# Optimization experiments

Measured on AMD Instinct MI355X. Metric: run time of the kernel, lower is better.

## Reference

```python
import jax, jax.numpy as jnp
import numpy as np

V = 5023   # FLAME vertex count
NJ = 5     # joints: global, neck, jaw, left eye, right eye
PARENTS = [-1, 0, 1, 1, 1]
N_SHAPE, N_EXPR = 100, 50
N_LMK = 68
B = 1024


def batch_rodrigues(rot_vecs):
    # rot_vecs: [N,3] axis-angle -> [N,3,3] rotation matrices
    angle = jnp.linalg.norm(rot_vecs + 1e-8, axis=1, keepdims=True)  # [N,1]
    rot_dir = rot_vecs / angle
    cos = jnp.cos(angle)[:, :, None]  # [N,1,1]
    sin = jnp.sin(angle)[:, :, None]
    rx, ry, rz = rot_dir[:, 0], rot_dir[:, 1], rot_dir[:, 2]
    zeros = jnp.zeros_like(rx)
    K = jnp.stack([zeros, -rz, ry,
                   rz, zeros, -rx,
                   -ry, rx, zeros], axis=1).reshape(-1, 3, 3)
    ident = jnp.eye(3, dtype=rot_vecs.dtype)
    return ident[None] + sin * K + (1.0 - cos) * jnp.matmul(K, K)


def setup_inputs() -> dict:
    key = jax.random.key(0)
    ks = jax.random.split(key, 12)
    shape_params = jax.random.normal(ks[0], (B, N_SHAPE), jnp.float32)
    expression_params = jax.random.normal(ks[1], (B, N_EXPR), jnp.float32)
    pose_params = 0.2 * jax.random.normal(ks[2], (B, 6), jnp.float32)
    land_index = jax.random.randint(ks[3], (N_LMK,), 0, V)
    # buffers / params (stand-ins for the pickled FLAME model)
    v_template = jax.random.normal(ks[4], (V, 3), jnp.float32) * 100.0
    v_template = v_template - jnp.mean(v_template, axis=0, keepdims=True)  # init centering
    shapedirs = jax.random.normal(ks[5], (V, 3, N_SHAPE + N_EXPR), jnp.float32) * 0.1
    posedirs = jax.random.normal(ks[6], ((NJ - 1) * 9, V * 3), jnp.float32) * 0.01
    J_regressor = jax.nn.softmax(jax.random.normal(ks[7], (NJ, V), jnp.float32), axis=1)
    lbs_weights = jax.nn.softmax(jax.random.normal(ks[8], (V, NJ), jnp.float32), axis=1)
    eye_pose = jnp.zeros((1, 6), jnp.float32)
    neck_pose = jnp.zeros((1, 3), jnp.float32)
    return dict(shape_params=shape_params, expression_params=expression_params,
                pose_params=pose_params, land_index=land_index,
                v_template=v_template, shapedirs=shapedirs, posedirs=posedirs,
                J_regressor=J_regressor, lbs_weights=lbs_weights,
                eye_pose=eye_pose, neck_pose=neck_pose)


def lbs(betas, full_pose, v_template, shapedirs, posedirs, J_regressor, lbs_weights):
    b = betas.shape[0]
    # shape/expression blendshapes
    v_shaped = v_template[None] + jnp.einsum('bl,vcl->bvc', betas, shapedirs)  # [B,V,3]
    J = jnp.einsum('jv,bvc->bjc', J_regressor, v_shaped)                       # [B,5,3]
    rot_mats = batch_rodrigues(full_pose.reshape(-1, 3)).reshape(b, NJ, 3, 3)
    ident = jnp.eye(3, dtype=betas.dtype)
    pose_feature = (rot_mats[:, 1:] - ident).reshape(b, -1)                    # [B,36]
    v_posed = v_shaped + jnp.matmul(pose_feature, posedirs).reshape(b, V, 3)
    # rigid transform along kinematic chain
    rel_joints = J.at[:, 1:].add(-J[:, jnp.array(PARENTS[1:])])
    top = jnp.concatenate([rot_mats, rel_joints[..., None]], axis=-1)          # [B,5,3,4]
    bottom = jnp.broadcast_to(jnp.array([0., 0., 0., 1.], betas.dtype), (b, NJ, 1, 4))
    transforms_mat = jnp.concatenate([top, bottom], axis=2)                    # [B,5,4,4]
    chain = [transforms_mat[:, 0]]
    for i in range(1, NJ):
        chain.append(jnp.matmul(chain[PARENTS[i]], transforms_mat[:, i]))
    transforms = jnp.stack(chain, axis=1)                                      # [B,5,4,4]
    posed_joints = transforms[:, :, :3, 3]
    t = jnp.einsum('bnij,bnj->bni', transforms[:, :, :3, :3], J)
    rel_transforms = transforms.at[:, :, :3, 3].add(-t)
    # skinning
    T = jnp.einsum('vj,bjxy->bvxy', lbs_weights, rel_transforms)               # [B,V,4,4]
    verts = jnp.einsum('bvxy,bvy->bvx', T[:, :, :3, :3], v_posed) + T[:, :, :3, 3]
    return verts, posed_joints


def reference(shape_params, expression_params, pose_params, land_index,
              v_template, shapedirs, posedirs, J_regressor, lbs_weights,
              eye_pose, neck_pose):
    b = shape_params.shape[0]
    betas = jnp.concatenate([shape_params, expression_params], axis=1)
    full_pose = jnp.concatenate([pose_params[:, :3],
                                 jnp.broadcast_to(neck_pose, (b, 3)),
                                 pose_params[:, 3:],
                                 jnp.broadcast_to(eye_pose, (b, 6))], axis=1)  # [B,15]
    vertices, _ = lbs(betas, full_pose, v_template, shapedirs, posedirs,
                      J_regressor, lbs_weights)
    landmarks3d = jnp.take(vertices, land_index, axis=1)
    return vertices, landmarks3d
```

## Files before the change

### kernel.cpp

```cpp
#include <hip/hip_runtime.h>

#define V_N 5023
#define NC_REAL 15069
#define NC_PAD 15168
#define KTOT 192
#define B_N 1024

__device__ __forceinline__ float bf2f(unsigned short u) {
  union { unsigned int i; float f; } x; x.i = ((unsigned int)u) << 16; return x.f;
}
__device__ __forceinline__ unsigned short f2bf(float f) {
  union { float f; unsigned int i; } x; x.f = f;
  unsigned int u = x.i;
  u = (u + 0x7FFFu + ((u >> 16) & 1u)) >> 16;
  return (unsigned short)u;
}

__global__ void k_sd_transpose(const float* __restrict__ sd,
                               unsigned short* __restrict__ sdT) {
  __shared__ unsigned short tile[64][153];
  int vc0 = blockIdx.x * 64;
  int t = threadIdx.x;
  int col = t >> 2, q = t & 3;
  int vc = vc0 + col;
  #pragma unroll
  for (int i = 0; i < 38; ++i) {
    int k = q * 38 + i;
    unsigned short val = 0;
    if (k < 150 && vc < NC_REAL) val = f2bf(sd[vc * 150 + k]);
    tile[col][k] = val;
  }
  __syncthreads();
  for (int u = t; u < 152 * 32; u += 256) {
    int row = u >> 5, cp = u & 31;
    unsigned int lo = tile[2 * cp][row], hi = tile[2 * cp + 1][row];
    ((unsigned int*)sdT)[row * (NC_PAD / 2) + (vc0 >> 1) + cp] = lo | (hi << 16);
  }
}

__global__ void k_pd_copy(const float* __restrict__ pd,
                          unsigned short* __restrict__ sdT) {
  int g = blockIdx.x * 256 + threadIdx.x;
  int rr = g / NC_PAD, vc = g - rr * NC_PAD;
  unsigned short val = 0;
  if (rr < 36 && vc < NC_REAL) val = f2bf(pd[rr * NC_REAL + vc]);
  sdT[(152 + rr) * NC_PAD + vc] = val;
}

__global__ void k_js(const float* __restrict__ jreg,
                     const float* __restrict__ sd,
                     const float* __restrict__ vt,
                     float* __restrict__ JS, float* __restrict__ Jt) {
  int blk = blockIdx.x;
  int t = threadIdx.x;
  float acc[5] = {0.f, 0.f, 0.f, 0.f, 0.f};
  if (blk < 450) {
    int c = blk / 150, l = blk - (blk / 150) * 150;
    for (int v = t; v < V_N; v += 256) {
      float s = sd[(v * 3 + c) * 150 + l];
      #pragma unroll
      for (int j = 0; j < 5; j++) acc[j] += jreg[j * V_N + v] * s;
    }
  } else {
    int c = blk - 450;
    for (int v = t; v < V_N; v += 256) {
      float s = vt[v * 3 + c];
      #pragma unroll
      for (int j = 0; j < 5; j++) acc[j] += jreg[j * V_N + v] * s;
    }
  }
  __shared__ float red[5][4];
  #pragma unroll
  for (int j = 0; j < 5; j++) {
    float x = acc[j];
    for (int off = 32; off > 0; off >>= 1) x += __shfl_down(x, off);
    if ((t & 63) == 0) red[j][t >> 6] = x;
  }
  __syncthreads();
  if (t < 5) {
    float s = red[t][0] + red[t][1] + red[t][2] + red[t][3];
    if (blk < 450) {
      int c = blk / 150, l = blk - (blk / 150) * 150;
      JS[(t * 3 + c) * 150 + l] = s;
    } else {
      Jt[t * 3 + (blk - 450)] = s;
    }
  }
}

__global__ void k_betasT(const float* __restrict__ shp,
                         const float* __restrict__ expr,
                         float* __restrict__ betasT) {
  int g = blockIdx.x * 256 + threadIdx.x;
  int k = g >> 10, b = g & 1023;
  float v = 0.f;
  if (k < 100) v = shp[b * 100 + k];
  else if (k < 150) v = expr[b * 50 + (k - 100)];
  betasT[g] = v;
}

__device__ __forceinline__ void rodrigues(const float* p, float* R) {
  float x = p[0], y = p[1], z = p[2];
  float xa = x + 1e-8f, ya = y + 1e-8f, za = z + 1e-8f;
  float angle = sqrtf(xa * xa + ya * ya + za * za);
  float inv = 1.0f / angle;
  float rx = x * inv, ry = y * inv, rz = z * inv;
  float c = cosf(angle), s = sinf(angle), t1 = 1.0f - c;
  float K[9] = {0.f, -rz, ry, rz, 0.f, -rx, -ry, rx, 0.f};
  float KK[9];
  #pragma unroll
  for (int i = 0; i < 3; i++)
    #pragma unroll
    for (int j = 0; j < 3; j++) {
      float a = 0.f;
      #pragma unroll
      for (int k = 0; k < 3; k++) a += K[i * 3 + k] * K[k * 3 + j];
      KK[i * 3 + j] = a;
    }
  #pragma unroll
  for (int i = 0; i < 9; i++) R[i] = s * K[i] + t1 * KK[i];
  R[0] += 1.f; R[4] += 1.f; R[8] += 1.f;
}

__global__ void k_pose(const float* __restrict__ pose,
                       const float* __restrict__ neck,
                       const float* __restrict__ eye,
                       const float* __restrict__ JS,
                       const float* __restrict__ Jt,
                       float* __restrict__ betasT,
                       float* __restrict__ relT) {
  int b = blockIdx.x * 256 + threadIdx.x;
  if (b >= B_N) return;
  float fp[15];
  fp[0] = pose[b * 6 + 0]; fp[1] = pose[b * 6 + 1]; fp[2] = pose[b * 6 + 2];
  fp[3] = neck[0]; fp[4] = neck[1]; fp[5] = neck[2];
  fp[6] = pose[b * 6 + 3]; fp[7] = pose[b * 6 + 4]; fp[8] = pose[b * 6 + 5];
  #pragma unroll
  for (int i = 0; i < 6; i++) fp[9 + i] = eye[i];
  float R[5][9];
  #pragma unroll
  for (int j = 0; j < 5; j++) rodrigues(&fp[j * 3], R[j]);
  float J[5][3];
  #pragma unroll
  for (int j = 0; j < 5; j++)
    #pragma unroll
    for (int c = 0; c < 3; c++) J[j][c] = Jt[j * 3 + c];
  for (int k = 0; k < 150; k++) {
    float be = betasT[k * B_N + b];
    #pragma unroll
    for (int j = 0; j < 5; j++)
      #pragma unroll
      for (int c = 0; c < 3; c++) J[j][c] += be * JS[(j * 3 + c) * 150 + k];
  }
  float rel[5][3];
  #pragma unroll
  for (int c = 0; c < 3; c++) {
    rel[0][c] = J[0][c];
    rel[1][c] = J[1][c] - J[0][c];
    rel[2][c] = J[2][c] - J[1][c];
    rel[3][c] = J[3][c] - J[1][c];
    rel[4][c] = J[4][c] - J[1][c];
  }
  float GR[5][9], Gt[5][3];
  #pragma unroll
  for (int i = 0; i < 9; i++) GR[0][i] = R[0][i];
  #pragma unroll
  for (int c = 0; c < 3; c++) Gt[0][c] = rel[0][c];
  const int parent[5] = {0, 0, 1, 1, 1};
  #pragma unroll
  for (int j = 1; j < 5; j++) {
    int p = parent[j];
    #pragma unroll
    for (int r = 0; r < 3; r++)
      #pragma unroll
      for (int c = 0; c < 3; c++) {
        float a = 0.f;
        #pragma unroll
        for (int k = 0; k < 3; k++) a += GR[p][r * 3 + k] * R[j][k * 3 + c];
        GR[j][r * 3 + c] = a;
      }
    #pragma unroll
    for (int r = 0; r < 3; r++) {
      float a = Gt[p][r];
      #pragma unroll
      for (int k = 0; k < 3; k++) a += GR[p][r * 3 + k] * rel[j][k];
      Gt[j][r] = a;
    }
  }
  #pragma unroll
  for (int j = 0; j < 5; j++) {
    #pragma unroll
    for (int r = 0; r < 3; r++) {
      float a = 0.f;
      #pragma unroll
      for (int k = 0; k < 3; k++) a += GR[j][r * 3 + k] * J[j][k];
      float tr = Gt[j][r] - a;
      #pragma unroll
      for (int c = 0; c < 3; c++) relT[b * 60 + j * 12 + r * 4 + c] = GR[j][r * 3 + c];
      relT[b * 60 + j * 12 + r * 4 + 3] = tr;
    }
  }
  #pragma unroll
  for (int j = 1; j < 5; j++)
    #pragma unroll
    for (int r = 0; r < 3; r++)
      #pragma unroll
      for (int c = 0; c < 3; c++) {
        int kk = (j - 1) * 9 + r * 3 + c;
        betasT[(152 + kk) * B_N + b] = R[j][r * 3 + c] - ((r == c) ? 1.f : 0.f);
      }
  #pragma unroll
  for (int kk = 36; kk < 40; kk++) betasT[(152 + kk) * B_N + b] = 0.f;
}

__global__ __launch_bounds__(256) void k_main(
    const unsigned short* __restrict__ sdT,
    const float* __restrict__ betasT,
    const float* __restrict__ relT,
    const float* __restrict__ vt,
    const float* __restrict__ lbsw,
    float* __restrict__ out) {
  __shared__ float sBet[8][64];
  __shared__ float sSd[8][3][64];
  int t = threadIdx.x;
  int bg = t >> 5;
  int tv = t & 31;
  int v0 = blockIdx.x * 64;
  int b0 = blockIdx.y * 64;
  float acc[8][2][3];
  #pragma unroll
  for (int a = 0; a < 8; a++)
    #pragma unroll
    for (int b2 = 0; b2 < 2; b2++)
      #pragma unroll
      for (int c = 0; c < 3; c++) acc[a][b2][c] = 0.f;
  const unsigned int* sdT32 = (const unsigned int*)sdT;
  for (int kc = 0; kc < 24; kc++) {
    int k0 = kc * 8;
    {
      int f = t;
      #pragma unroll
      for (int i = 0; i < 2; i++, f += 256) {
        int r = f >> 6, c = f & 63;
        sBet[r][c] = betasT[(k0 + r) * B_N + b0 + c];
      }
      int u = t;
      #pragma unroll
      for (int i = 0; i < 3; i++, u += 256) {
        int r = u / 96, c2 = u - (u / 96) * 96;
        unsigned int w = sdT32[(k0 + r) * (NC_PAD / 2) + blockIdx.x * 96 + c2];
        int vcA = 2 * c2, vcB = vcA + 1;
        sSd[r][vcA % 3][vcA / 3] = bf2f((unsigned short)(w & 0xFFFFu));
        sSd[r][vcB % 3][vcB / 3] = bf2f((unsigned short)(w >> 16));
      }
    }
    __syncthreads();
    #pragma unroll
    for (int r = 0; r < 8; r++) {
      float4 be0 = *(const float4*)&sBet[r][bg * 8];
      float4 be1 = *(const float4*)&sBet[r][bg * 8 + 4];
      float2 sx = *(const float2*)&sSd[r][0][2 * tv];
      float2 sy = *(const float2*)&sSd[r][1][2 * tv];
      float2 sz = *(const float2*)&sSd[r][2][2 * tv];
      float be[8] = {be0.x, be0.y, be0.z, be0.w, be1.x, be1.y, be1.z, be1.w};
      #pragma unroll
      for (int bi = 0; bi < 8; bi++) {
        acc[bi][0][0] += be[bi] * sx.x;
        acc[bi][1][0] += be[bi] * sx.y;
        acc[bi][0][1] += be[bi] * sy.x;
        acc[bi][1][1] += be[bi] * sy.y;
        acc[bi][0][2] += be[bi] * sz.x;
        acc[bi][1][2] += be[bi] * sz.y;
      }
    }
    __syncthreads();
  }
  int vA = v0 + 2 * tv, vB = vA + 1;
  bool okA = vA < V_N, okB = vB < V_N;
  float vtA[3] = {0.f, 0.f, 0.f}, vtB[3] = {0.f, 0.f, 0.f};
  float wA[5] = {0.f, 0.f, 0.f, 0.f, 0.f}, wB[5] = {0.f, 0.f, 0.f, 0.f, 0.f};
  if (okA) {
    #pragma unroll
    for (int c = 0; c < 3; c++) vtA[c] = vt[vA * 3 + c];
    #pragma unroll
    for (int j = 0; j < 5; j++) wA[j] = lbsw[vA * 5 + j];
  }
  if (okB) {
    #pragma unroll
    for (int c = 0; c < 3; c++) vtB[c] = vt[vB * 3 + c];
    #pragma unroll
    for (int j = 0; j < 5; j++) wB[j] = lbsw[vB * 5 + j];
  }
  #pragma unroll
  for (int bi = 0; bi < 8; bi++) {
    int b = b0 + bg * 8 + bi;
    const float4* rT = (const float4*)(relT + b * 60);
    float pA0 = acc[bi][0][0] + vtA[0], pA1 = acc[bi][0][1] + vtA[1], pA2 = acc[bi][0][2] + vtA[2];
    float pB0 = acc[bi][1][0] + vtB[0], pB1 = acc[bi][1][1] + vtB[1], pB2 = acc[bi][1][2] + vtB[2];
    float oA0 = 0.f, oA1 = 0.f, oA2 = 0.f, oB0 = 0.f, oB1 = 0.f, oB2 = 0.f;
    #pragma unroll
    for (int j = 0; j < 5; j++) {
      float4 m0 = rT[j * 3 + 0], m1 = rT[j * 3 + 1], m2 = rT[j * 3 + 2];
      oA0 += wA[j] * (m0.x * pA0 + m0.y * pA1 + m0.z * pA2 + m0.w);
      oA1 += wA[j] * (m1.x * pA0 + m1.y * pA1 + m1.z * pA2 + m1.w);
      oA2 += wA[j] * (m2.x * pA0 + m2.y * pA1 + m2.z * pA2 + m2.w);
      oB0 += wB[j] * (m0.x * pB0 + m0.y * pB1 + m0.z * pB2 + m0.w);
      oB1 += wB[j] * (m1.x * pB0 + m1.y * pB1 + m1.z * pB2 + m1.w);
      oB2 += wB[j] * (m2.x * pB0 + m2.y * pB1 + m2.z * pB2 + m2.w);
    }
    if (okA) {
      size_t off = (size_t)b * NC_REAL + (size_t)vA * 3;
      out[off] = oA0; out[off + 1] = oA1; out[off + 2] = oA2;
    }
    if (okB) {
      size_t off = (size_t)b * NC_REAL + (size_t)vB * 3;
      out[off] = oB0; out[off + 1] = oB1; out[off + 2] = oB2;
    }
  }
}

__global__ void k_lmk(const float* __restrict__ verts,
                      const int* __restrict__ land,
                      float* __restrict__ lm) {
  int g = blockIdx.x * 256 + threadIdx.x;
  int b = g / 204;
  int r = g - b * 204;
  int i = r / 3, c = r - i * 3;
  lm[g] = verts[(size_t)b * NC_REAL + (size_t)land[i] * 3 + c];
}

extern "C" void kernel_launch(void* const* d_in, const int* in_sizes, int n_in,
                              void* d_out, int out_size, void* d_ws, size_t ws_size,
                              hipStream_t stream) {
  const float* shp  = (const float*)d_in[0];
  const float* expr = (const float*)d_in[1];
  const float* pose = (const float*)d_in[2];
  const int*   land = (const int*)d_in[3];
  const float* vt   = (const float*)d_in[4];
  const float* sd   = (const float*)d_in[5];
  const float* pd   = (const float*)d_in[6];
  const float* jreg = (const float*)d_in[7];
  const float* lbsw = (const float*)d_in[8];
  const float* eye  = (const float*)d_in[9];
  const float* neck = (const float*)d_in[10];
  char* ws = (char*)d_ws;
  unsigned short* sdT = (unsigned short*)(ws + 0);
  float* betasT = (float*)(ws + 5824512);
  float* JS     = (float*)(ws + 6610944);
  float* Jt     = (float*)(ws + 6620160);
  float* relT   = (float*)(ws + 6620224);
  float* outv = (float*)d_out;
  float* outl = outv + (size_t)B_N * NC_REAL;

  hipLaunchKernelGGL(k_sd_transpose, dim3(237), dim3(256), 0, stream, sd, sdT);
  hipLaunchKernelGGL(k_pd_copy, dim3(2370), dim3(256), 0, stream, pd, sdT);
  hipLaunchKernelGGL(k_js, dim3(453), dim3(256), 0, stream, jreg, sd, vt, JS, Jt);
  hipLaunchKernelGGL(k_betasT, dim3(608), dim3(256), 0, stream, shp, expr, betasT);
  hipLaunchKernelGGL(k_pose, dim3(4), dim3(256), 0, stream, pose, neck, eye, JS, Jt, betasT, relT);
  hipLaunchKernelGGL(k_main, dim3(79, 16), dim3(256), 0, stream, sdT, betasT, relT, vt, lbsw, outv);
  hipLaunchKernelGGL(k_lmk, dim3(816), dim3(256), 0, stream, outv, land, outl);
}
```

Baseline: 274.9 us.

## Move blendshape GEMM to bf16 MFMA and restructure preprocessing kernels

```diff
diff --git a/kernel.cpp b/kernel.cpp
--- a/kernel.cpp
+++ b/kernel.cpp
@@ -1,14 +1,22 @@
 #include <hip/hip_runtime.h>
 
 #define V_N 5023
-#define NC_REAL 15069
-#define NC_PAD 15168
+#define V_PAD 5120
 #define KTOT 192
 #define B_N 1024
-
-__device__ __forceinline__ float bf2f(unsigned short u) {
-  union { unsigned int i; float f; } x; x.i = ((unsigned int)u) << 16; return x.f;
-}
+#define NC_REAL 15069
+
+#define WS_W     0
+#define WS_A2    5898240
+#define WS_PART1 6291456
+#define WS_PARTJ 6561456
+#define WS_JS    6563264
+#define WS_JT    6572272
+#define WS_RELT  6572336
+
+typedef __attribute__((ext_vector_type(8))) short bf16x8;
+typedef __attribute__((ext_vector_type(4))) float f32x4;
+
 __device__ __forceinline__ unsigned short f2bf(float f) {
   union { float f; unsigned int i; } x; x.f = f;
   unsigned int u = x.i;
@@ -16,87 +24,82 @@
   return (unsigned short)u;
 }
 
-__global__ void k_sd_transpose(const float* __restrict__ sd,
-                               unsigned short* __restrict__ sdT) {
-  __shared__ unsigned short tile[64][153];
-  int vc0 = blockIdx.x * 64;
-  int t = threadIdx.x;
-  int col = t >> 2, q = t & 3;
-  int vc = vc0 + col;
-  #pragma unroll
-  for (int i = 0; i < 38; ++i) {
-    int k = q * 38 + i;
-    unsigned short val = 0;
-    if (k < 150 && vc < NC_REAL) val = f2bf(sd[vc * 150 + k]);
-    tile[col][k] = val;
-  }
-  __syncthreads();
-  for (int u = t; u < 152 * 32; u += 256) {
-    int row = u >> 5, cp = u & 31;
-    unsigned int lo = tile[2 * cp][row], hi = tile[2 * cp + 1][row];
-    ((unsigned int*)sdT)[row * (NC_PAD / 2) + (vc0 >> 1) + cp] = lo | (hi << 16);
-  }
-}
-
-__global__ void k_pd_copy(const float* __restrict__ pd,
-                          unsigned short* __restrict__ sdT) {
+__global__ void k_w2(const float* __restrict__ sd, const float* __restrict__ pd,
+                     unsigned short* __restrict__ W) {
+  int vc = blockIdx.x * 256 + threadIdx.x;
+  int v = vc / 3, c = vc - 3 * v;
+  unsigned short* dst = W + ((size_t)c * V_PAD + v) * KTOT;
+  if (vc < NC_REAL) {
+    for (int k = 0; k < 150; k++) dst[k] = f2bf(sd[(size_t)vc * 150 + k]);
+    dst[150] = 0; dst[151] = 0;
+    for (int kk = 0; kk < 36; kk++) dst[152 + kk] = f2bf(pd[(size_t)kk * NC_REAL + vc]);
+    for (int k = 188; k < 192; k++) dst[k] = 0;
+  } else {
+    for (int k = 0; k < 192; k++) dst[k] = 0;
+  }
+}
+
+__global__ void k_a2(const float* __restrict__ shp, const float* __restrict__ expr,
+                     unsigned short* __restrict__ A2) {
   int g = blockIdx.x * 256 + threadIdx.x;
-  int rr = g / NC_PAD, vc = g - rr * NC_PAD;
-  unsigned short val = 0;
-  if (rr < 36 && vc < NC_REAL) val = f2bf(pd[rr * NC_REAL + vc]);
-  sdT[(152 + rr) * NC_PAD + vc] = val;
-}
-
-__global__ void k_js(const float* __restrict__ jreg,
-                     const float* __restrict__ sd,
-                     const float* __restrict__ vt,
-                     float* __restrict__ JS, float* __restrict__ Jt) {
+  int b = g / 76, u = g - b * 76;
+  int k0 = 2 * u, k1 = 2 * u + 1;
+  float f0 = 0.f, f1 = 0.f;
+  if (k0 < 100) f0 = shp[b * 100 + k0]; else if (k0 < 150) f0 = expr[b * 50 + k0 - 100];
+  if (k1 < 100) f1 = shp[b * 100 + k1]; else if (k1 < 150) f1 = expr[b * 50 + k1 - 100];
+  unsigned int w = (unsigned int)f2bf(f0) | ((unsigned int)f2bf(f1) << 16);
+  ((unsigned int*)A2)[b * 96 + u] = w;
+}
+
+__global__ void k_js1(const float* __restrict__ jreg, const float* __restrict__ sd,
+                      const float* __restrict__ vt,
+                      float* __restrict__ part1, float* __restrict__ partJ) {
   int blk = blockIdx.x;
   int t = threadIdx.x;
-  float acc[5] = {0.f, 0.f, 0.f, 0.f, 0.f};
-  if (blk < 450) {
-    int c = blk / 150, l = blk - (blk / 150) * 150;
-    for (int v = t; v < V_N; v += 256) {
-      float s = sd[(v * 3 + c) * 150 + l];
-      #pragma unroll
-      for (int j = 0; j < 5; j++) acc[j] += jreg[j * V_N + v] * s;
-    }
-  } else {
-    int c = blk - 450;
-    for (int v = t; v < V_N; v += 256) {
-      float s = vt[v * 3 + c];
-      #pragma unroll
-      for (int j = 0; j < 5; j++) acc[j] += jreg[j * V_N + v] * s;
-    }
-  }
-  __shared__ float red[5][4];
-  #pragma unroll
-  for (int j = 0; j < 5; j++) {
-    float x = acc[j];
-    for (int off = 32; off > 0; off >>= 1) x += __shfl_down(x, off);
-    if ((t & 63) == 0) red[j][t >> 6] = x;
-  }
-  __syncthreads();
-  if (t < 5) {
-    float s = red[t][0] + red[t][1] + red[t][2] + red[t][3];
-    if (blk < 450) {
-      int c = blk / 150, l = blk - (blk / 150) * 150;
-      JS[(t * 3 + c) * 150 + l] = s;
-    } else {
-      Jt[t * 3 + (blk - 450)] = s;
-    }
-  }
-}
-
-__global__ void k_betasT(const float* __restrict__ shp,
-                         const float* __restrict__ expr,
-                         float* __restrict__ betasT) {
-  int g = blockIdx.x * 256 + threadIdx.x;
-  int k = g >> 10, b = g & 1023;
-  float v = 0.f;
-  if (k < 100) v = shp[b * 100 + k];
-  else if (k < 150) v = expr[b * 50 + (k - 100)];
-  betasT[g] = v;
+  int vs = blk * 168, ve = vs + 168; if (ve > V_N) ve = V_N;
+  if (t < 150) {
+    float acc[5][3];
+    #pragma unroll
+    for (int j = 0; j < 5; j++)
+      #pragma unroll
+      for (int c = 0; c < 3; c++) acc[j][c] = 0.f;
+    for (int v = vs; v < ve; v++) {
+      float jr[5];
+      #pragma unroll
+      for (int j = 0; j < 5; j++) jr[j] = jreg[j * V_N + v];
+      #pragma unroll
+      for (int c = 0; c < 3; c++) {
+        float s = sd[(size_t)(3 * v + c) * 150 + t];
+        #pragma unroll
+        for (int j = 0; j < 5; j++) acc[j][c] += jr[j] * s;
+      }
+    }
+    #pragma unroll
+    for (int j = 0; j < 5; j++)
+      #pragma unroll
+      for (int c = 0; c < 3; c++)
+        part1[(size_t)blk * 2250 + (j * 3 + c) * 150 + t] = acc[j][c];
+  } else if (t >= 160 && t < 175) {
+    int j = (t - 160) / 3, c = (t - 160) % 3;
+    float a = 0.f;
+    for (int v = vs; v < ve; v++) a += jreg[j * V_N + v] * vt[3 * v + c];
+    partJ[blk * 15 + (t - 160)] = a;
+  }
+}
+
+__global__ void k_js2(const float* __restrict__ part1, const float* __restrict__ partJ,
+                      float* __restrict__ JS, float* __restrict__ Jt) {
+  int t = threadIdx.x;
+  for (int u = t; u < 2250; u += 256) {
+    float s = 0.f;
+    for (int blk = 0; blk < 30; blk++) s += part1[(size_t)blk * 2250 + u];
+    JS[u] = s;
+  }
+  if (t < 15) {
+    float s = 0.f;
+    for (int blk = 0; blk < 30; blk++) s += partJ[blk * 15 + t];
+    Jt[t] = s;
+  }
 }
 
 __device__ __forceinline__ void rodrigues(const float* p, float* R) {
@@ -125,12 +128,13 @@
 __global__ void k_pose(const float* __restrict__ pose,
                        const float* __restrict__ neck,
                        const float* __restrict__ eye,
+                       const float* __restrict__ shp,
+                       const float* __restrict__ expr,
                        const float* __restrict__ JS,
                        const float* __restrict__ Jt,
-                       float* __restrict__ betasT,
+                       unsigned short* __restrict__ A2,
                        float* __restrict__ relT) {
-  int b = blockIdx.x * 256 + threadIdx.x;
-  if (b >= B_N) return;
+  int b = blockIdx.x * 64 + threadIdx.x;
   float fp[15];
   fp[0] = pose[b * 6 + 0]; fp[1] = pose[b * 6 + 1]; fp[2] = pose[b * 6 + 2];
   fp[3] = neck[0]; fp[4] = neck[1]; fp[5] = neck[2];
@@ -146,7 +150,7 @@
     #pragma unroll
     for (int c = 0; c < 3; c++) J[j][c] = Jt[j * 3 + c];
   for (int k = 0; k < 150; k++) {
-    float be = betasT[k * B_N + b];
+    float be = (k < 100) ? shp[b * 100 + k] : expr[b * 50 + k - 100];
     #pragma unroll
     for (int j = 0; j < 5; j++)
       #pragma unroll
@@ -207,115 +211,102 @@
       #pragma unroll
       for (int c = 0; c < 3; c++) {
         int kk = (j - 1) * 9 + r * 3 + c;
-        betasT[(152 + kk) * B_N + b] = R[j][r * 3 + c] - ((r == c) ? 1.f : 0.f);
-      }
-  #pragma unroll
-  for (int kk = 36; kk < 40; kk++) betasT[(152 + kk) * B_N + b] = 0.f;
-}
-
-__global__ __launch_bounds__(256) void k_main(
-    const unsigned short* __restrict__ sdT,
-    const float* __restrict__ betasT,
+        A2[(size_t)b * KTOT + 152 + kk] = f2bf(R[j][r * 3 + c] - ((r == c) ? 1.f : 0.f));
+      }
+  #pragma unroll
+  for (int kk = 36; kk < 40; kk++) A2[(size_t)b * KTOT + 152 + kk] = 0;
+}
+
+__global__ __launch_bounds__(256) void k_mfma(
+    const unsigned short* __restrict__ W,
+    const unsigned short* __restrict__ A2,
     const float* __restrict__ relT,
     const float* __restrict__ vt,
     const float* __restrict__ lbsw,
     float* __restrict__ out) {
-  __shared__ float sBet[8][64];
-  __shared__ float sSd[8][3][64];
+  __shared__ unsigned short sA[64 * 40];
+  __shared__ unsigned short sB[3 * 128 * 40];
+  __shared__ float sRel[64 * 60];
   int t = threadIdx.x;
-  int bg = t >> 5;
-  int tv = t & 31;
-  int v0 = blockIdx.x * 64;
-  int b0 = blockIdx.y * 64;
-  float acc[8][2][3];
-  #pragma unroll
-  for (int a = 0; a < 8; a++)
-    #pragma unroll
-    for (int b2 = 0; b2 < 2; b2++)
-      #pragma unroll
-      for (int c = 0; c < 3; c++) acc[a][b2][c] = 0.f;
-  const unsigned int* sdT32 = (const unsigned int*)sdT;
-  for (int kc = 0; kc < 24; kc++) {
-    int k0 = kc * 8;
+  int wave = t >> 6, lane = t & 63, ln = lane & 15, quad = lane >> 4;
+  int wm = wave >> 1, wn = wave & 1;
+  int v0 = blockIdx.x * 128, b0 = blockIdx.y * 64;
+
+  for (int i = t; i < 3840; i += 256) sRel[i] = relT[(size_t)b0 * 60 + i];
+
+  f32x4 acc[3][2][4];
+  #pragma unroll
+  for (int c = 0; c < 3; c++)
+    #pragma unroll
+    for (int mt = 0; mt < 2; mt++)
+      #pragma unroll
+      for (int nt = 0; nt < 4; nt++) {
+        acc[c][mt][nt].x = 0.f; acc[c][mt][nt].y = 0.f;
+        acc[c][mt][nt].z = 0.f; acc[c][mt][nt].w = 0.f;
+      }
+
+  for (int kc = 0; kc < 6; kc++) {
     {
-      int f = t;
-      #pragma unroll
-      for (int i = 0; i < 2; i++, f += 256) {
-        int r = f >> 6, c = f & 63;
-        sBet[r][c] = betasT[(k0 + r) * B_N + b0 + c];
-      }
-      int u = t;
-      #pragma unroll
-      for (int i = 0; i < 3; i++, u += 256) {
-        int r = u / 96, c2 = u - (u / 96) * 96;
-        unsigned int w = sdT32[(k0 + r) * (NC_PAD / 2) + blockIdx.x * 96 + c2];
-        int vcA = 2 * c2, vcB = vcA + 1;
-        sSd[r][vcA % 3][vcA / 3] = bf2f((unsigned short)(w & 0xFFFFu));
-        sSd[r][vcB % 3][vcB / 3] = bf2f((unsigned short)(w >> 16));
-      }
+      int row = t >> 2, part = t & 3;
+      const float4* src = (const float4*)(A2 + (size_t)(b0 + row) * KTOT + kc * 32 + part * 8);
+      *(float4*)&sA[row * 40 + part * 8] = *src;
+    }
+    #pragma unroll
+    for (int i = 0; i < 6; i++) {
+      int task = i * 256 + t;
+      int row = task >> 2, part = task & 3;
+      int c = row >> 7, n = row & 127;
+      const float4* src = (const float4*)(W + ((size_t)c * V_PAD + v0 + n) * KTOT + kc * 32 + part * 8);
+      *(float4*)&sB[(c * 128 + n) * 40 + part * 8] = *src;
     }
     __syncthreads();
-    #pragma unroll
-    for (int r = 0; r < 8; r++) {
-      float4 be0 = *(const float4*)&sBet[r][bg * 8];
-      float4 be1 = *(const float4*)&sBet[r][bg * 8 + 4];
-      float2 sx = *(const float2*)&sSd[r][0][2 * tv];
-      float2 sy = *(const float2*)&sSd[r][1][2 * tv];
-      float2 sz = *(const float2*)&sSd[r][2][2 * tv];
-      float be[8] = {be0.x, be0.y, be0.z, be0.w, be1.x, be1.y, be1.z, be1.w};
-      #pragma unroll
-      for (int bi = 0; bi < 8; bi++) {
-        acc[bi][0][0] += be[bi] * sx.x;
-        acc[bi][1][0] += be[bi] * sx.y;
-        acc[bi][0][1] += be[bi] * sy.x;
-        acc[bi][1][1] += be[bi] * sy.y;
-        acc[bi][0][2] += be[bi] * sz.x;
-        acc[bi][1][2] += be[bi] * sz.y;
-      }
-    }
+    bf16x8 af0 = *(const bf16x8*)&sA[(wm * 32 + ln) * 40 + quad * 8];
+    bf16x8 af1 = *(const bf16x8*)&sA[(wm * 32 + 16 + ln) * 40 + quad * 8];
+    #pragma unroll
+    for (int c = 0; c < 3; c++)
+      #pragma unroll
+      for (int nt = 0; nt < 4; nt++) {
+        bf16x8 bf = *(const bf16x8*)&sB[(c * 128 + wn * 64 + nt * 16 + ln) * 40 + quad * 8];
+        acc[c][0][nt] = __builtin_amdgcn_mfma_f32_16x16x32_bf16(af0, bf, acc[c][0][nt], 0, 0, 0);
+        acc[c][1][nt] = __builtin_amdgcn_mfma_f32_16x16x32_bf16(af1, bf, acc[c][1][nt], 0, 0, 0);
+      }
     __syncthreads();
   }
-  int vA = v0 + 2 * tv, vB = vA + 1;
-  bool okA = vA < V_N, okB = vB < V_N;
-  float vtA[3] = {0.f, 0.f, 0.f}, vtB[3] = {0.f, 0.f, 0.f};
-  float wA[5] = {0.f, 0.f, 0.f, 0.f, 0.f}, wB[5] = {0.f, 0.f, 0.f, 0.f, 0.f};
-  if (okA) {
-    #pragma unroll
-    for (int c = 0; c < 3; c++) vtA[c] = vt[vA * 3 + c];
-    #pragma unroll
-    for (int j = 0; j < 5; j++) wA[j] = lbsw[vA * 5 + j];
-  }
-  if (okB) {
-    #pragma unroll
-    for (int c = 0; c < 3; c++) vtB[c] = vt[vB * 3 + c];
-    #pragma unroll
-    for (int j = 0; j < 5; j++) wB[j] = lbsw[vB * 5 + j];
-  }
-  #pragma unroll
-  for (int bi = 0; bi < 8; bi++) {
-    int b = b0 + bg * 8 + bi;
-    const float4* rT = (const float4*)(relT + b * 60);
-    float pA0 = acc[bi][0][0] + vtA[0], pA1 = acc[bi][0][1] + vtA[1], pA2 = acc[bi][0][2] + vtA[2];
-    float pB0 = acc[bi][1][0] + vtB[0], pB1 = acc[bi][1][1] + vtB[1], pB2 = acc[bi][1][2] + vtB[2];
-    float oA0 = 0.f, oA1 = 0.f, oA2 = 0.f, oB0 = 0.f, oB1 = 0.f, oB2 = 0.f;
-    #pragma unroll
-    for (int j = 0; j < 5; j++) {
-      float4 m0 = rT[j * 3 + 0], m1 = rT[j * 3 + 1], m2 = rT[j * 3 + 2];
-      oA0 += wA[j] * (m0.x * pA0 + m0.y * pA1 + m0.z * pA2 + m0.w);
-      oA1 += wA[j] * (m1.x * pA0 + m1.y * pA1 + m1.z * pA2 + m1.w);
-      oA2 += wA[j] * (m2.x * pA0 + m2.y * pA1 + m2.z * pA2 + m2.w);
-      oB0 += wB[j] * (m0.x * pB0 + m0.y * pB1 + m0.z * pB2 + m0.w);
-      oB1 += wB[j] * (m1.x * pB0 + m1.y * pB1 + m1.z * pB2 + m1.w);
-      oB2 += wB[j] * (m2.x * pB0 + m2.y * pB1 + m2.z * pB2 + m2.w);
-    }
-    if (okA) {
-      size_t off = (size_t)b * NC_REAL + (size_t)vA * 3;
-      out[off] = oA0; out[off + 1] = oA1; out[off + 2] = oA2;
-    }
-    if (okB) {
-      size_t off = (size_t)b * NC_REAL + (size_t)vB * 3;
-      out[off] = oB0; out[off + 1] = oB1; out[off + 2] = oB2;
-    }
+
+  #pragma unroll
+  for (int nt = 0; nt < 4; nt++) {
+    int v = v0 + wn * 64 + nt * 16 + ln;
+    bool ok = v < V_N;
+    float vtx = 0.f, vty = 0.f, vtz = 0.f;
+    float w5[5] = {0.f, 0.f, 0.f, 0.f, 0.f};
+    if (ok) {
+      vtx = vt[3 * v]; vty = vt[3 * v + 1]; vtz = vt[3 * v + 2];
+      #pragma unroll
+      for (int j = 0; j < 5; j++) w5[j] = lbsw[v * 5 + j];
+    }
+    #pragma unroll
+    for (int mt = 0; mt < 2; mt++)
+      #pragma unroll
+      for (int reg = 0; reg < 4; reg++) {
+        int bl = wm * 32 + mt * 16 + quad * 4 + reg;
+        float px = acc[0][mt][nt][reg] + vtx;
+        float py = acc[1][mt][nt][reg] + vty;
+        float pz = acc[2][mt][nt][reg] + vtz;
+        float ox = 0.f, oy = 0.f, oz = 0.f;
+        const float* M = &sRel[bl * 60];
+        #pragma unroll
+        for (int j = 0; j < 5; j++) {
+          const float* m = M + j * 12;
+          float q0 = m[0] * px + m[1] * py + m[2] * pz + m[3];
+          float q1 = m[4] * px + m[5] * py + m[6] * pz + m[7];
+          float q2 = m[8] * px + m[9] * py + m[10] * pz + m[11];
+          ox += w5[j] * q0; oy += w5[j] * q1; oz += w5[j] * q2;
+        }
+        if (ok) {
+          size_t off = (size_t)(b0 + bl) * NC_REAL + (size_t)3 * v;
+          out[off] = ox; out[off + 1] = oy; out[off + 2] = oz;
+        }
+      }
   }
 }
 
@@ -344,19 +335,21 @@
   const float* eye  = (const float*)d_in[9];
   const float* neck = (const float*)d_in[10];
   char* ws = (char*)d_ws;
-  unsigned short* sdT = (unsigned short*)(ws + 0);
-  float* betasT = (float*)(ws + 5824512);
-  float* JS     = (float*)(ws + 6610944);
-  float* Jt     = (float*)(ws + 6620160);
-  float* relT   = (float*)(ws + 6620224);
+  unsigned short* W    = (unsigned short*)(ws + WS_W);
+  unsigned short* A2   = (unsigned short*)(ws + WS_A2);
+  float* part1 = (float*)(ws + WS_PART1);
+  float* partJ = (float*)(ws + WS_PARTJ);
+  float* JS    = (float*)(ws + WS_JS);
+  float* Jt    = (float*)(ws + WS_JT);
+  float* relT  = (float*)(ws + WS_RELT);
   float* outv = (float*)d_out;
   float* outl = outv + (size_t)B_N * NC_REAL;
 
-  hipLaunchKernelGGL(k_sd_transpose, dim3(237), dim3(256), 0, stream, sd, sdT);
-  hipLaunchKernelGGL(k_pd_copy, dim3(2370), dim3(256), 0, stream, pd, sdT);
-  hipLaunchKernelGGL(k_js, dim3(453), dim3(256), 0, stream, jreg, sd, vt, JS, Jt);
-  hipLaunchKernelGGL(k_betasT, dim3(608), dim3(256), 0, stream, shp, expr, betasT);
-  hipLaunchKernelGGL(k_pose, dim3(4), dim3(256), 0, stream, pose, neck, eye, JS, Jt, betasT, relT);
-  hipLaunchKernelGGL(k_main, dim3(79, 16), dim3(256), 0, stream, sdT, betasT, relT, vt, lbsw, outv);
-  hipLaunchKernelGGL(k_lmk, dim3(816), dim3(256), 0, stream, outv, land, outl);
-}
+  hipLaunchKernelGGL(k_w2,   dim3(60),      dim3(256), 0, stream, sd, pd, W);
+  hipLaunchKernelGGL(k_a2,   dim3(304),     dim3(256), 0, stream, shp, expr, A2);
+  hipLaunchKernelGGL(k_js1,  dim3(30),      dim3(256), 0, stream, jreg, sd, vt, part1, partJ);
+  hipLaunchKernelGGL(k_js2,  dim3(1),       dim3(256), 0, stream, part1, partJ, JS, Jt);
+  hipLaunchKernelGGL(k_pose, dim3(16),      dim3(64),  0, stream, pose, neck, eye, shp, expr, JS, Jt, A2, relT);
+  hipLaunchKernelGGL(k_mfma, dim3(40, 16),  dim3(256), 0, stream, W, A2, relT, vt, lbsw, outv);
+  hipLaunchKernelGGL(k_lmk,  dim3(816),     dim3(256), 0, stream, outv, land, outl);
+}
```

New measurement: 309.0 us. +12.4%, slower.
